# Kernel optimization log

Hardware: AMD Instinct MI355X
Metric: run time of the kernel (lower is better)

Reference implementation:

```python
import jax, jax.numpy as jnp
import numpy as np

GAMMA = 2.0
EPS = 1e-06
LAMBDA_DISTANCE = 1.0
LAMBDA_NORMAL = 0.01
LAMBDA_LAPLACIAN = 0.1
CLS = 1


def vertex_normals(v, f, eps=EPS):
    # v: [N,3], f: [F,3] int. Scatter face normals to vertices, then normalize.
    fv = v[f]  # [F,3,3]
    fn = jnp.cross(fv[:, 1] - fv[:, 0], fv[:, 2] - fv[:, 0])  # [F,3]
    vn = jnp.zeros_like(v)
    vn = vn.at[f[:, 0]].add(fn).at[f[:, 1]].add(fn).at[f[:, 2]].add(fn)
    norm = jnp.maximum(jnp.linalg.norm(vn, axis=-1, keepdims=True), eps)
    return vn / norm


def squared_cdist(a, b):
    # [Na,3] x [Nb,3] -> squared euclidean distances [Na,Nb] (clamped >= 0)
    a2 = jnp.sum(a * a, axis=1)[:, None]
    b2 = jnp.sum(b * b, axis=1)[None, :]
    d2 = a2 + b2 - 2.0 * (a @ b.T)
    return jnp.maximum(d2, 0.0)


def sample_binary_targets(label, v, cls=CLS):
    # Nearest-neighbor grid_sample, align_corners=True, padding zeros.
    # grid = 2*v - 1 -> voxel index = round(v * (size-1)); v[:,0]->W, v[:,1]->H, v[:,2]->D.
    D, H, W = label.shape[2], label.shape[3], label.shape[4]
    ix = jnp.round(v[:, 0] * (W - 1)).astype(jnp.int32)
    iy = jnp.round(v[:, 1] * (H - 1)).astype(jnp.int32)
    iz = jnp.round(v[:, 2] * (D - 1)).astype(jnp.int32)
    inb = (ix >= 0) & (ix < W) & (iy >= 0) & (iy < H) & (iz >= 0) & (iz < D)
    ixc = jnp.clip(ix, 0, W - 1)
    iyc = jnp.clip(iy, 0, H - 1)
    izc = jnp.clip(iz, 0, D - 1)
    vals = (label[0, 0, izc, iyc, ixc] == cls).astype(jnp.float32)
    return jnp.where(inb, vals, 0.0)


def spatial_consistency_loss(rel_pos, targets, gamma=GAMMA, eps=EPS):
    p = jnp.clip(rel_pos, eps, 1.0 - eps)
    pos = targets > 0.5
    pc = jnp.sum(pos).astype(p.dtype)
    tot = jnp.asarray(p.shape[0], p.dtype)
    nc = tot - pc
    alpha = nc / (tot + eps)
    lpos = -alpha * jnp.power(1.0 - p, gamma) * jnp.log(p)
    lneg = -(1.0 - alpha) * jnp.power(p, gamma) * jnp.log(1.0 - p)
    return jnp.sum(jnp.where(pos, lpos, lneg)) / (tot + eps)


def laplacian_uniform(v, f):
    # Uniform mesh Laplacian smoothing: || mean(neighbors) - v ||, averaged.
    i = jnp.concatenate([f[:, 0], f[:, 1], f[:, 2], f[:, 1], f[:, 2], f[:, 0]])
    j = jnp.concatenate([f[:, 1], f[:, 2], f[:, 0], f[:, 0], f[:, 1], f[:, 2]])
    nsum = jnp.zeros_like(v).at[i].add(v[j])
    deg = jnp.zeros((v.shape[0],), v.dtype).at[i].add(1.0)
    lap = nsum / jnp.maximum(deg, 1.0)[:, None] - v
    return jnp.mean(jnp.linalg.norm(lap, axis=1))


def loss_forward(pred_vertices, relative_positions, gt_vertices, pred_faces, gt_faces, label):
    gt_v = jax.lax.stop_gradient(gt_vertices)  # gt comes from label volume; detached in original
    gt_normals = vertex_normals(gt_v, gt_faces)
    # spatial (focal-style) loss
    targets = sample_binary_targets(label, pred_vertices)
    spatial = spatial_consistency_loss(relative_positions, targets)
    # chamfer-style squared surface distance
    d2 = squared_cdist(pred_vertices, gt_v)  # [Np,Ng]
    distance = jnp.mean(jnp.min(d2, axis=1)) + jnp.mean(jnp.min(d2, axis=0))
    # normal consistency vs nearest gt vertex
    pred_normals = vertex_normals(pred_vertices, pred_faces)
    nearest = jnp.argmin(d2, axis=1)
    normal = jnp.mean((pred_normals - gt_normals[nearest]) ** 2)
    # uniform laplacian smoothing
    laplacian = laplacian_uniform(pred_vertices, pred_faces)
    total = spatial + LAMBDA_DISTANCE * distance + LAMBDA_NORMAL * normal + LAMBDA_LAPLACIAN * laplacian
    return total


def setup_inputs() -> dict:
    key = jax.random.key(0)
    k1, k2, k3, k4, k5, k6 = jax.random.split(key, 6)
    Np, Ng = 8192, 12000
    pred_vertices = jax.random.uniform(k1, (Np, 3), dtype=jnp.float32)
    relative_positions = jax.random.uniform(k2, (Np,), dtype=jnp.float32)
    gt_vertices = jax.random.uniform(k3, (Ng, 3), dtype=jnp.float32)
    pred_faces = jax.random.randint(k4, (2 * Np, 3), 0, Np, dtype=jnp.int32)
    gt_faces = jax.random.randint(k5, (2 * Ng, 3), 0, Ng, dtype=jnp.int32)
    label = jax.random.randint(k6, (1, 1, 96, 96, 96), 0, 2, dtype=jnp.int32)
    return {"pred_vertices": pred_vertices, "relative_positions": relative_positions,
            "gt_vertices": gt_vertices, "pred_faces": pred_faces,
            "gt_faces": gt_faces, "label": label}


def reference(pred_vertices, relative_positions, gt_vertices, pred_faces, gt_faces, label):
    return loss_forward(pred_vertices, relative_positions, gt_vertices, pred_faces, gt_faces, label)
```

## Files before the change

kernel.cpp:

```cpp
#include <hip/hip_runtime.h>
#include <math.h>

#define NP 8192
#define NG 12000
#define NFP 16384
#define NFG 24000
#define EPSF 1e-6f

#define GR 16
#define NC (GR*GR*GR)
#define HCELL 0.0625f
#define QL 16
#define QPB (256 / QL)
#define PRED_QBLOCKS (NP / QPB)
#define GT_QBLOCKS (NG / QPB)
#define FIN_TOTAL (PRED_QBLOCKS + GT_QBLOCKS)

static constexpr size_t OFF_STARTP = 0;
static constexpr size_t OFF_CURP   = 16640;
static constexpr size_t OFF_STARTG = 33024;
static constexpr size_t OFF_CURG   = 49664;
static constexpr size_t OFF_SORTP  = 66048;
static constexpr size_t OFF_SORTG  = 197120;
static constexpr size_t OFF_GTN    = 389120;
static constexpr size_t OFF_PNN    = 533120;
static constexpr size_t OFF_NSUM   = 631424;
static constexpr size_t OFF_DEG    = 729728;
static constexpr size_t OFF_PART   = 762496;
#define N_ZERO 93344

__device__ __forceinline__ int cell_of(float x) {
    int c = (int)(x * (float)GR);
    return min(max(c, 0), GR - 1);
}

__device__ __forceinline__ void hist_scan(const float* __restrict__ pts, int n,
                                          unsigned* __restrict__ start,
                                          unsigned* __restrict__ cur,
                                          unsigned* h, unsigned* ps) {
    int t = threadIdx.x;
    for (int i = t; i < NC; i += 1024) h[i] = 0u;
    __syncthreads();
    for (int i = t; i < n; i += 1024) {
        int c = (cell_of(pts[3*i+2]) * GR + cell_of(pts[3*i+1])) * GR + cell_of(pts[3*i]);
        atomicAdd(&h[c], 1u);
    }
    __syncthreads();
    unsigned a0 = h[4*t], a1 = h[4*t+1], a2 = h[4*t+2], a3 = h[4*t+3];
    unsigned tsum = a0 + a1 + a2 + a3;
    ps[t] = tsum; __syncthreads();
    for (int off = 1; off < 1024; off <<= 1) {
        unsigned v = (t >= off) ? ps[t - off] : 0u;
        __syncthreads();
        ps[t] += v;
        __syncthreads();
    }
    unsigned ex = ps[t] - tsum;
    h[4*t] = ex; h[4*t+1] = ex + a0; h[4*t+2] = ex + a0 + a1; h[4*t+3] = ex + a0 + a1 + a2;
    __syncthreads();
    for (int i = t; i < NC; i += 1024) { start[i] = h[i]; cur[i] = h[i]; }
    if (t == 0) start[NC] = (unsigned)n;
}

__global__ __launch_bounds__(1024) void build_kernel(const float* __restrict__ pred,
                                                     const float* __restrict__ gt,
                                                     unsigned* __restrict__ startP,
                                                     unsigned* __restrict__ curP,
                                                     unsigned* __restrict__ startG,
                                                     unsigned* __restrict__ curG,
                                                     float* __restrict__ zero) {
    __shared__ unsigned h[NC];
    __shared__ unsigned ps[1024];
    if (blockIdx.x == 0) {
        hist_scan(pred, NP, startP, curP, h, ps);
    } else if (blockIdx.x == 1) {
        hist_scan(gt, NG, startG, curG, h, ps);
    } else {
        int i = (blockIdx.x - 2) * 1024 + threadIdx.x;
        if (i < N_ZERO) zero[i] = 0.0f;
    }
}

#define SCAT_P_BLOCKS 32
#define SCAT_G_BLOCKS 47
#define SCAT_BLOCKS (SCAT_P_BLOCKS + SCAT_G_BLOCKS)
#define FACE_BLOCKS ((NFG + NFP + 255) / 256)
__global__ __launch_bounds__(256) void scatter_faces_kernel(const float* __restrict__ pred,
                                                            const int* __restrict__ pf,
                                                            const float* __restrict__ gt,
                                                            const int* __restrict__ gf,
                                                            unsigned* __restrict__ curP,
                                                            unsigned* __restrict__ curG,
                                                            float4* __restrict__ sortP,
                                                            float4* __restrict__ sortG,
                                                            float* __restrict__ gtn,
                                                            float* __restrict__ pnn,
                                                            float* __restrict__ nsum,
                                                            float* __restrict__ deg) {
    int b = blockIdx.x;
    if (b < SCAT_P_BLOCKS) {
        int i = b * 256 + threadIdx.x;
        float x = pred[3*i], y = pred[3*i+1], z = pred[3*i+2];
        int c = (cell_of(z) * GR + cell_of(y)) * GR + cell_of(x);
        unsigned pos = atomicAdd(&curP[c], 1u);
        sortP[pos] = make_float4(x, y, z, __int_as_float(i));
    } else if (b < SCAT_BLOCKS) {
        int i = (b - SCAT_P_BLOCKS) * 256 + threadIdx.x;
        if (i < NG) {
            float x = gt[3*i], y = gt[3*i+1], z = gt[3*i+2];
            int c = (cell_of(z) * GR + cell_of(y)) * GR + cell_of(x);
            unsigned pos = atomicAdd(&curG[c], 1u);
            sortG[pos] = make_float4(x, y, z, __int_as_float(i));
        }
    } else {
        int t = (b - SCAT_BLOCKS) * 256 + threadIdx.x;
        if (t < NFG) {
            int i0 = gf[3*t], i1 = gf[3*t+1], i2 = gf[3*t+2];
            float ax = gt[3*i0], ay = gt[3*i0+1], az = gt[3*i0+2];
            float bx = gt[3*i1], by = gt[3*i1+1], bz = gt[3*i1+2];
            float cx = gt[3*i2], cy = gt[3*i2+1], cz = gt[3*i2+2];
            float ux = bx-ax, uy = by-ay, uz = bz-az;
            float wx = cx-ax, wy = cy-ay, wz = cz-az;
            float nx = uy*wz - uz*wy, ny = uz*wx - ux*wz, nz = ux*wy - uy*wx;
            atomicAdd(&gtn[3*i0+0], nx); atomicAdd(&gtn[3*i0+1], ny); atomicAdd(&gtn[3*i0+2], nz);
            atomicAdd(&gtn[3*i1+0], nx); atomicAdd(&gtn[3*i1+1], ny); atomicAdd(&gtn[3*i1+2], nz);
            atomicAdd(&gtn[3*i2+0], nx); atomicAdd(&gtn[3*i2+1], ny); atomicAdd(&gtn[3*i2+2], nz);
        } else if (t < NFG + NFP) {
            int u = t - NFG;
            int i0 = pf[3*u], i1 = pf[3*u+1], i2 = pf[3*u+2];
            float ax = pred[3*i0], ay = pred[3*i0+1], az = pred[3*i0+2];
            float bx = pred[3*i1], by = pred[3*i1+1], bz = pred[3*i1+2];
            float cx = pred[3*i2], cy = pred[3*i2+1], cz = pred[3*i2+2];
            float ux = bx-ax, uy = by-ay, uz = bz-az;
            float wx = cx-ax, wy = cy-ay, wz = cz-az;
            float nx = uy*wz - uz*wy, ny = uz*wx - ux*wz, nz = ux*wy - uy*wx;
            atomicAdd(&pnn[3*i0+0], nx); atomicAdd(&pnn[3*i0+1], ny); atomicAdd(&pnn[3*i0+2], nz);
            atomicAdd(&pnn[3*i1+0], nx); atomicAdd(&pnn[3*i1+1], ny); atomicAdd(&pnn[3*i1+2], nz);
            atomicAdd(&pnn[3*i2+0], nx); atomicAdd(&pnn[3*i2+1], ny); atomicAdd(&pnn[3*i2+2], nz);
            atomicAdd(&nsum[3*i0+0], bx+cx); atomicAdd(&nsum[3*i0+1], by+cy); atomicAdd(&nsum[3*i0+2], bz+cz);
            atomicAdd(&nsum[3*i1+0], cx+ax); atomicAdd(&nsum[3*i1+1], cy+ay); atomicAdd(&nsum[3*i1+2], cz+az);
            atomicAdd(&nsum[3*i2+0], ax+bx); atomicAdd(&nsum[3*i2+1], ay+by); atomicAdd(&nsum[3*i2+2], az+bz);
            atomicAdd(&deg[i0], 2.0f); atomicAdd(&deg[i1], 2.0f); atomicAdd(&deg[i2], 2.0f);
        }
    }
}

__device__ __forceinline__ float wave_sum(float x) {
    #pragma unroll
    for (int o = 32; o > 0; o >>= 1) x += __shfl_down(x, o, 64);
    return x;
}

__device__ __forceinline__ unsigned long long u64min(unsigned long long a,
                                                     unsigned long long b) {
    return a < b ? a : b;
}

__device__ __forceinline__ unsigned long long group_nn(int lane,
                                                       float px, float py, float pz,
                                                       const float4* __restrict__ S,
                                                       const unsigned* __restrict__ cstart) {
    int cx = cell_of(px), cy = cell_of(py), cz = cell_of(pz);
    unsigned long long best = 0xFFFFFFFFFFFFFFFFULL;
    for (int r = 1; ; ++r) {
        int w = 2 * r + 1;
        int nrows = w * w;
        int x0 = max(cx - r, 0), x1 = min(cx + r, GR - 1);
        unsigned long long lb = 0xFFFFFFFFFFFFFFFFULL;
        for (int k = lane; k < nrows; k += QL) {
            int z = cz + k / w - r, y = cy + k % w - r;
            if (z >= 0 && z < GR && y >= 0 && y < GR) {
                int rowbase = (z * GR + y) * GR;
                unsigned s0 = cstart[rowbase + x0];
                unsigned s1 = cstart[rowbase + x1 + 1];
                for (unsigned t = s0; t < s1; ++t) {
                    float4 q = S[t];
                    float ddx = px - q.x, ddy = py - q.y, ddz = pz - q.z;
                    float d2 = fmaf(ddx, ddx, fmaf(ddy, ddy, ddz*ddz));
                    unsigned long long key =
                        ((unsigned long long)__float_as_uint(d2) << 32) |
                        (unsigned)__float_as_int(q.w);
                    lb = u64min(lb, key);
                }
            }
        }
        best = u64min(best, lb);
        #pragma unroll
        for (int m = 1; m < QL; m <<= 1)
            best = u64min(best, (unsigned long long)__shfl_xor((long long)best, m, 64));
        bool covered = (cx - r <= 0) & (cx + r >= GR - 1) &
                       (cy - r <= 0) & (cy + r >= GR - 1) &
                       (cz - r <= 0) & (cz + r >= GR - 1);
        if (covered) break;
        float blo = 1.0e30f;
        if (cx - r > 0)      blo = fminf(blo, px - (float)(cx - r) * HCELL);
        if (cx + r < GR - 1) blo = fminf(blo, (float)(cx + r + 1) * HCELL - px);
        if (cy - r > 0)      blo = fminf(blo, py - (float)(cy - r) * HCELL);
        if (cy + r < GR - 1) blo = fminf(blo, (float)(cy + r + 1) * HCELL - py);
        if (cz - r > 0)      blo = fminf(blo, pz - (float)(cz - r) * HCELL);
        if (cz + r < GR - 1) blo = fminf(blo, (float)(cz + r + 1) * HCELL - pz);
        float bd2 = __uint_as_float((unsigned)(best >> 32));
        if (bd2 <= blo * blo) break;
    }
    return best;
}

__global__ __launch_bounds__(256) void query_kernel(const float* __restrict__ relpos,
                                                    const int* __restrict__ label,
                                                    const float4* __restrict__ sortP,
                                                    const float4* __restrict__ sortG,
                                                    const unsigned* __restrict__ startP,
                                                    const unsigned* __restrict__ startG,
                                                    const float* __restrict__ pnn,
                                                    const float* __restrict__ gtn,
                                                    const float* __restrict__ nsum,
                                                    const float* __restrict__ deg,
                                                    float* __restrict__ partial) {
    __shared__ float bsum[6];
    if (threadIdx.x < 6) bsum[threadIdx.x] = 0.0f;
    __syncthreads();
    int lane = threadIdx.x & (QL - 1);
    int group = threadIdx.x >> 4;
    if (blockIdx.x < PRED_QBLOCKS) {
        int qid = blockIdx.x * QPB + group;
        float4 P = sortP[qid];
        float px = P.x, py = P.y, pz = P.z;
        unsigned long long key = group_nn(lane, px, py, pz, sortG, startG);

        float r0 = 0.f, r1 = 0.f, r2 = 0.f, r3 = 0.f, r4 = 0.f, r5 = 0.f;
        if (lane == 0) {
            int v = __float_as_int(P.w);
            float dmin = __uint_as_float((unsigned)(key >> 32));
            int nearest = (int)(unsigned)(key & 0xffffffffu);

            float ax = pnn[3*v], ay = pnn[3*v+1], az = pnn[3*v+2];
            float an = fmaxf(sqrtf(ax*ax + ay*ay + az*az), EPSF);
            float gx = gtn[3*nearest], gy = gtn[3*nearest+1], gz = gtn[3*nearest+2];
            float gn = fmaxf(sqrtf(gx*gx + gy*gy + gz*gz), EPSF);
            float nx = ax/an - gx/gn, ny = ay/an - gy/gn, nz = az/an - gz/gn;
            float sse = nx*nx + ny*ny + nz*nz;

            float d = fmaxf(deg[v], 1.0f);
            float lx = nsum[3*v]/d - px, ly = nsum[3*v+1]/d - py, lz = nsum[3*v+2]/d - pz;
            float lapn = sqrtf(lx*lx + ly*ly + lz*lz);

            int ix = (int)rintf(px * 95.0f), iy = (int)rintf(py * 95.0f), iz = (int)rintf(pz * 95.0f);
            bool inb = (ix >= 0) & (ix < 96) & (iy >= 0) & (iy < 96) & (iz >= 0) & (iz < 96);
            int ixc = min(max(ix, 0), 95), iyc = min(max(iy, 0), 95), izc = min(max(iz, 0), 95);
            bool pos = inb && (label[(izc*96 + iyc)*96 + ixc] == 1);

            float p = fminf(fmaxf(relpos[v], EPSF), 1.0f - EPSF);
            float om = 1.0f - p;
            float pcnt = 0.0f, sx = 0.0f, sy = 0.0f;
            if (pos) { pcnt = 1.0f; sx = om*om*logf(p); }
            else     { sy = p*p*logf(om); }

            r0 = dmin; r1 = sse; r2 = lapn; r3 = pcnt; r4 = sx; r5 = sy;
        }
        r0 = wave_sum(r0); r1 = wave_sum(r1); r2 = wave_sum(r2);
        r3 = wave_sum(r3); r4 = wave_sum(r4); r5 = wave_sum(r5);
        if ((threadIdx.x & 63) == 0) {
            atomicAdd(&bsum[0], r0); atomicAdd(&bsum[1], r1);
            atomicAdd(&bsum[2], r2); atomicAdd(&bsum[3], r3);
            atomicAdd(&bsum[4], r4); atomicAdd(&bsum[5], r5);
        }
        __syncthreads();
        if (threadIdx.x < 6)
            partial[(size_t)blockIdx.x * 8 + threadIdx.x] = bsum[threadIdx.x];
    } else {
        int qid = (blockIdx.x - PRED_QBLOCKS) * QPB + group;
        float4 Q = sortG[qid];
        unsigned long long key = group_nn(lane, Q.x, Q.y, Q.z, sortP, startP);
        float val = (lane == 0) ? __uint_as_float((unsigned)(key >> 32)) : 0.0f;
        float r = wave_sum(val);
        if ((threadIdx.x & 63) == 0) atomicAdd(&bsum[0], r);
        __syncthreads();
        if (threadIdx.x == 0)
            partial[(size_t)blockIdx.x * 8] = bsum[0];
    }
}

__global__ __launch_bounds__(256) void combine_kernel(const float* __restrict__ partial,
                                                      float* __restrict__ out) {
    float s0=0.f, s1=0.f, s2=0.f, s3=0.f, s4=0.f, s5=0.f, s6=0.f;
    for (int r = threadIdx.x; r < FIN_TOTAL; r += 256) {
        const float* p = partial + (size_t)r * 8;
        if (r < PRED_QBLOCKS) {
            s0 += p[0]; s1 += p[1]; s2 += p[2];
            s3 += p[3]; s4 += p[4]; s5 += p[5];
        } else {
            s6 += p[0];
        }
    }
    s0 = wave_sum(s0); s1 = wave_sum(s1); s2 = wave_sum(s2); s3 = wave_sum(s3);
    s4 = wave_sum(s4); s5 = wave_sum(s5); s6 = wave_sum(s6);
    __shared__ float acc[7];
    if (threadIdx.x < 7) acc[threadIdx.x] = 0.0f;
    __syncthreads();
    if ((threadIdx.x & 63) == 0) {
        atomicAdd(&acc[0], s0); atomicAdd(&acc[1], s1); atomicAdd(&acc[2], s2);
        atomicAdd(&acc[3], s3); atomicAdd(&acc[4], s4); atomicAdd(&acc[5], s5);
        atomicAdd(&acc[6], s6);
    }
    __syncthreads();
    if (threadIdx.x == 0) {
        float sum_row = acc[0], sse = acc[1], lap = acc[2];
        float pc = acc[3], SX = acc[4], SY = acc[5], sum_col = acc[6];
        float tot = (float)NP;
        float alpha = (tot - pc) / (tot + EPSF);
        float spatial = (-alpha * SX - (1.0f - alpha) * SY) / (tot + EPSF);
        float distance = sum_row / (float)NP + sum_col / (float)NG;
        float normal = sse / (float)(NP * 3);
        float lapm = lap / (float)NP;
        out[0] = spatial + 1.0f * distance + 0.01f * normal + 0.1f * lapm;
    }
}

extern "C" void kernel_launch(void* const* d_in, const int* in_sizes, int n_in,
                              void* d_out, int out_size, void* d_ws, size_t ws_size,
                              hipStream_t stream) {
    const float* pred   = (const float*)d_in[0];
    const float* relpos = (const float*)d_in[1];
    const float* gt     = (const float*)d_in[2];
    const int*   pfaces = (const int*)d_in[3];
    const int*   gfaces = (const int*)d_in[4];
    const int*   label  = (const int*)d_in[5];
    float* out = (float*)d_out;

    char* ws = (char*)d_ws;
    unsigned* startP  = (unsigned*)(ws + OFF_STARTP);
    unsigned* curP    = (unsigned*)(ws + OFF_CURP);
    unsigned* startG  = (unsigned*)(ws + OFF_STARTG);
    unsigned* curG    = (unsigned*)(ws + OFF_CURG);
    float4*   sortP   = (float4*)(ws + OFF_SORTP);
    float4*   sortG   = (float4*)(ws + OFF_SORTG);
    float*    gtn     = (float*)(ws + OFF_GTN);
    float*    pnn     = (float*)(ws + OFF_PNN);
    float*    nsum    = (float*)(ws + OFF_NSUM);
    float*    deg     = (float*)(ws + OFF_DEG);
    float*    partial = (float*)(ws + OFF_PART);

    int zero_blocks = (N_ZERO + 1023) / 1024;
    hipLaunchKernelGGL(build_kernel, dim3(2 + zero_blocks), dim3(1024), 0, stream,
                       pred, gt, startP, curP, startG, curG, gtn);
    hipLaunchKernelGGL(scatter_faces_kernel, dim3(SCAT_BLOCKS + FACE_BLOCKS), dim3(256), 0, stream,
                       pred, pfaces, gt, gfaces, curP, curG, sortP, sortG,
                       gtn, pnn, nsum, deg);
    hipLaunchKernelGGL(query_kernel, dim3(FIN_TOTAL), dim3(256), 0, stream,
                       relpos, label, sortP, sortG, startP, startG,
                       pnn, gtn, nsum, deg, partial);
    hipLaunchKernelGGL(combine_kernel, dim3(1), dim3(256), 0, stream, partial, out);
}
```

Measured before the change: 116.3 us.

## Restructure pipeline: scatter in build kernel, overlap face normals with NN queries

The point-to-cell scatter moves into the single-block histogram kernel, using shared-memory atomics on the scanned offsets. Face-normal and Laplacian accumulation now run in the same launch as the nearest-neighbour queries, so the separate scatter kernel goes away. Pred queries only store their NN keys, and a single-block finalize kernel computes the per-vertex normal, Laplacian and focal terms and reduces everything. This cuts the chain from four launches to three, at the cost of serializing the scatter inside one block per cloud and doing 8192 vertex finalizations in one 256-thread block.

After: 176.4 us. 51.6% more time.

```diff
diff --git a/kernel.cpp b/kernel.cpp
--- a/kernel.cpp
+++ b/kernel.cpp
@@ -14,19 +14,17 @@
 #define QPB (256 / QL)
 #define PRED_QBLOCKS (NP / QPB)
 #define GT_QBLOCKS (NG / QPB)
-#define FIN_TOTAL (PRED_QBLOCKS + GT_QBLOCKS)
 
 static constexpr size_t OFF_STARTP = 0;
-static constexpr size_t OFF_CURP   = 16640;
-static constexpr size_t OFF_STARTG = 33024;
-static constexpr size_t OFF_CURG   = 49664;
-static constexpr size_t OFF_SORTP  = 66048;
-static constexpr size_t OFF_SORTG  = 197120;
-static constexpr size_t OFF_GTN    = 389120;
-static constexpr size_t OFF_PNN    = 533120;
-static constexpr size_t OFF_NSUM   = 631424;
-static constexpr size_t OFF_DEG    = 729728;
-static constexpr size_t OFF_PART   = 762496;
+static constexpr size_t OFF_STARTG = 16640;
+static constexpr size_t OFF_SORTP  = 33280;
+static constexpr size_t OFF_SORTG  = 164352;
+static constexpr size_t OFF_KEYS   = 356352;
+static constexpr size_t OFF_COLP   = 421888;
+static constexpr size_t OFF_GTN    = 424960;
+static constexpr size_t OFF_PNN    = 568960;
+static constexpr size_t OFF_NSUM   = 667264;
+static constexpr size_t OFF_DEG    = 765568;
 #define N_ZERO 93344
 
 __device__ __forceinline__ int cell_of(float x) {
@@ -34,10 +32,10 @@
     return min(max(c, 0), GR - 1);
 }
 
-__device__ __forceinline__ void hist_scan(const float* __restrict__ pts, int n,
-                                          unsigned* __restrict__ start,
-                                          unsigned* __restrict__ cur,
-                                          unsigned* h, unsigned* ps) {
+__device__ __forceinline__ void hist_scan_scatter(const float* __restrict__ pts, int n,
+                                                  unsigned* __restrict__ start,
+                                                  float4* __restrict__ sorted,
+                                                  unsigned* h, unsigned* ps) {
     int t = threadIdx.x;
     for (int i = t; i < NC; i += 1024) h[i] = 0u;
     __syncthreads();
@@ -58,90 +56,33 @@
     unsigned ex = ps[t] - tsum;
     h[4*t] = ex; h[4*t+1] = ex + a0; h[4*t+2] = ex + a0 + a1; h[4*t+3] = ex + a0 + a1 + a2;
     __syncthreads();
-    for (int i = t; i < NC; i += 1024) { start[i] = h[i]; cur[i] = h[i]; }
+    for (int i = t; i < NC; i += 1024) start[i] = h[i];
     if (t == 0) start[NC] = (unsigned)n;
+    __syncthreads();
+    for (int i = t; i < n; i += 1024) {
+        float x = pts[3*i], y = pts[3*i+1], z = pts[3*i+2];
+        int c = (cell_of(z) * GR + cell_of(y)) * GR + cell_of(x);
+        unsigned pos = atomicAdd(&h[c], 1u);
+        sorted[pos] = make_float4(x, y, z, __int_as_float(i));
+    }
 }
 
 __global__ __launch_bounds__(1024) void build_kernel(const float* __restrict__ pred,
                                                      const float* __restrict__ gt,
                                                      unsigned* __restrict__ startP,
-                                                     unsigned* __restrict__ curP,
                                                      unsigned* __restrict__ startG,
-                                                     unsigned* __restrict__ curG,
+                                                     float4* __restrict__ sortP,
+                                                     float4* __restrict__ sortG,
                                                      float* __restrict__ zero) {
     __shared__ unsigned h[NC];
     __shared__ unsigned ps[1024];
     if (blockIdx.x == 0) {
-        hist_scan(pred, NP, startP, curP, h, ps);
+        hist_scan_scatter(pred, NP, startP, sortP, h, ps);
     } else if (blockIdx.x == 1) {
-        hist_scan(gt, NG, startG, curG, h, ps);
+        hist_scan_scatter(gt, NG, startG, sortG, h, ps);
     } else {
         int i = (blockIdx.x - 2) * 1024 + threadIdx.x;
         if (i < N_ZERO) zero[i] = 0.0f;
-    }
-}
-
-#define SCAT_P_BLOCKS 32
-#define SCAT_G_BLOCKS 47
-#define SCAT_BLOCKS (SCAT_P_BLOCKS + SCAT_G_BLOCKS)
-#define FACE_BLOCKS ((NFG + NFP + 255) / 256)
-__global__ __launch_bounds__(256) void scatter_faces_kernel(const float* __restrict__ pred,
-                                                            const int* __restrict__ pf,
-                                                            const float* __restrict__ gt,
-                                                            const int* __restrict__ gf,
-                                                            unsigned* __restrict__ curP,
-                                                            unsigned* __restrict__ curG,
-                                                            float4* __restrict__ sortP,
-                                                            float4* __restrict__ sortG,
-                                                            float* __restrict__ gtn,
-                                                            float* __restrict__ pnn,
-                                                            float* __restrict__ nsum,
-                                                            float* __restrict__ deg) {
-    int b = blockIdx.x;
-    if (b < SCAT_P_BLOCKS) {
-        int i = b * 256 + threadIdx.x;
-        float x = pred[3*i], y = pred[3*i+1], z = pred[3*i+2];
-        int c = (cell_of(z) * GR + cell_of(y)) * GR + cell_of(x);
-        unsigned pos = atomicAdd(&curP[c], 1u);
-        sortP[pos] = make_float4(x, y, z, __int_as_float(i));
-    } else if (b < SCAT_BLOCKS) {
-        int i = (b - SCAT_P_BLOCKS) * 256 + threadIdx.x;
-        if (i < NG) {
-            float x = gt[3*i], y = gt[3*i+1], z = gt[3*i+2];
-            int c = (cell_of(z) * GR + cell_of(y)) * GR + cell_of(x);
-            unsigned pos = atomicAdd(&curG[c], 1u);
-            sortG[pos] = make_float4(x, y, z, __int_as_float(i));
-        }
-    } else {
-        int t = (b - SCAT_BLOCKS) * 256 + threadIdx.x;
-        if (t < NFG) {
-            int i0 = gf[3*t], i1 = gf[3*t+1], i2 = gf[3*t+2];
-            float ax = gt[3*i0], ay = gt[3*i0+1], az = gt[3*i0+2];
-            float bx = gt[3*i1], by = gt[3*i1+1], bz = gt[3*i1+2];
-            float cx = gt[3*i2], cy = gt[3*i2+1], cz = gt[3*i2+2];
-            float ux = bx-ax, uy = by-ay, uz = bz-az;
-            float wx = cx-ax, wy = cy-ay, wz = cz-az;
-            float nx = uy*wz - uz*wy, ny = uz*wx - ux*wz, nz = ux*wy - uy*wx;
-            atomicAdd(&gtn[3*i0+0], nx); atomicAdd(&gtn[3*i0+1], ny); atomicAdd(&gtn[3*i0+2], nz);
-            atomicAdd(&gtn[3*i1+0], nx); atomicAdd(&gtn[3*i1+1], ny); atomicAdd(&gtn[3*i1+2], nz);
-            atomicAdd(&gtn[3*i2+0], nx); atomicAdd(&gtn[3*i2+1], ny); atomicAdd(&gtn[3*i2+2], nz);
-        } else if (t < NFG + NFP) {
-            int u = t - NFG;
-            int i0 = pf[3*u], i1 = pf[3*u+1], i2 = pf[3*u+2];
-            float ax = pred[3*i0], ay = pred[3*i0+1], az = pred[3*i0+2];
-            float bx = pred[3*i1], by = pred[3*i1+1], bz = pred[3*i1+2];
-            float cx = pred[3*i2], cy = pred[3*i2+1], cz = pred[3*i2+2];
-            float ux = bx-ax, uy = by-ay, uz = bz-az;
-            float wx = cx-ax, wy = cy-ay, wz = cz-az;
-            float nx = uy*wz - uz*wy, ny = uz*wx - ux*wz, nz = ux*wy - uy*wx;
-            atomicAdd(&pnn[3*i0+0], nx); atomicAdd(&pnn[3*i0+1], ny); atomicAdd(&pnn[3*i0+2], nz);
-            atomicAdd(&pnn[3*i1+0], nx); atomicAdd(&pnn[3*i1+1], ny); atomicAdd(&pnn[3*i1+2], nz);
-            atomicAdd(&pnn[3*i2+0], nx); atomicAdd(&pnn[3*i2+1], ny); atomicAdd(&pnn[3*i2+2], nz);
-            atomicAdd(&nsum[3*i0+0], bx+cx); atomicAdd(&nsum[3*i0+1], by+cy); atomicAdd(&nsum[3*i0+2], bz+cz);
-            atomicAdd(&nsum[3*i1+0], cx+ax); atomicAdd(&nsum[3*i1+1], cy+ay); atomicAdd(&nsum[3*i1+2], cz+az);
-            atomicAdd(&nsum[3*i2+0], ax+bx); atomicAdd(&nsum[3*i2+1], ay+by); atomicAdd(&nsum[3*i2+2], az+bz);
-            atomicAdd(&deg[i0], 2.0f); atomicAdd(&deg[i1], 2.0f); atomicAdd(&deg[i2], 2.0f);
-        }
     }
 }
 
@@ -205,113 +146,139 @@
     return best;
 }
 
-__global__ __launch_bounds__(256) void query_kernel(const float* __restrict__ relpos,
-                                                    const int* __restrict__ label,
-                                                    const float4* __restrict__ sortP,
-                                                    const float4* __restrict__ sortG,
-                                                    const unsigned* __restrict__ startP,
-                                                    const unsigned* __restrict__ startG,
-                                                    const float* __restrict__ pnn,
-                                                    const float* __restrict__ gtn,
-                                                    const float* __restrict__ nsum,
-                                                    const float* __restrict__ deg,
-                                                    float* __restrict__ partial) {
-    __shared__ float bsum[6];
-    if (threadIdx.x < 6) bsum[threadIdx.x] = 0.0f;
-    __syncthreads();
-    int lane = threadIdx.x & (QL - 1);
-    int group = threadIdx.x >> 4;
-    if (blockIdx.x < PRED_QBLOCKS) {
-        int qid = blockIdx.x * QPB + group;
+#define FACE_BLOCKS ((NFG + NFP + 255) / 256)
+#define D2_BLOCKS (FACE_BLOCKS + PRED_QBLOCKS + GT_QBLOCKS)
+__global__ __launch_bounds__(256) void work_kernel(const float* __restrict__ pred,
+                                                   const int* __restrict__ pf,
+                                                   const float* __restrict__ gt,
+                                                   const int* __restrict__ gf,
+                                                   const float4* __restrict__ sortP,
+                                                   const float4* __restrict__ sortG,
+                                                   const unsigned* __restrict__ startP,
+                                                   const unsigned* __restrict__ startG,
+                                                   unsigned long long* __restrict__ keys,
+                                                   float* __restrict__ colpart,
+                                                   float* __restrict__ gtn,
+                                                   float* __restrict__ pnn,
+                                                   float* __restrict__ nsum,
+                                                   float* __restrict__ deg) {
+    int b = blockIdx.x;
+    if (b < FACE_BLOCKS) {
+        int t = b * 256 + threadIdx.x;
+        if (t < NFG) {
+            int i0 = gf[3*t], i1 = gf[3*t+1], i2 = gf[3*t+2];
+            float ax = gt[3*i0], ay = gt[3*i0+1], az = gt[3*i0+2];
+            float bx = gt[3*i1], by = gt[3*i1+1], bz = gt[3*i1+2];
+            float cx = gt[3*i2], cy = gt[3*i2+1], cz = gt[3*i2+2];
+            float ux = bx-ax, uy = by-ay, uz = bz-az;
+            float wx = cx-ax, wy = cy-ay, wz = cz-az;
+            float nx = uy*wz - uz*wy, ny = uz*wx - ux*wz, nz = ux*wy - uy*wx;
+            atomicAdd(&gtn[3*i0+0], nx); atomicAdd(&gtn[3*i0+1], ny); atomicAdd(&gtn[3*i0+2], nz);
+            atomicAdd(&gtn[3*i1+0], nx); atomicAdd(&gtn[3*i1+1], ny); atomicAdd(&gtn[3*i1+2], nz);
+            atomicAdd(&gtn[3*i2+0], nx); atomicAdd(&gtn[3*i2+1], ny); atomicAdd(&gtn[3*i2+2], nz);
+        } else if (t < NFG + NFP) {
+            int u = t - NFG;
+            int i0 = pf[3*u], i1 = pf[3*u+1], i2 = pf[3*u+2];
+            float ax = pred[3*i0], ay = pred[3*i0+1], az = pred[3*i0+2];
+            float bx = pred[3*i1], by = pred[3*i1+1], bz = pred[3*i1+2];
+            float cx = pred[3*i2], cy = pred[3*i2+1], cz = pred[3*i2+2];
+            float ux = bx-ax, uy = by-ay, uz = bz-az;
+            float wx = cx-ax, wy = cy-ay, wz = cz-az;
+            float nx = uy*wz - uz*wy, ny = uz*wx - ux*wz, nz = ux*wy - uy*wx;
+            atomicAdd(&pnn[3*i0+0], nx); atomicAdd(&pnn[3*i0+1], ny); atomicAdd(&pnn[3*i0+2], nz);
+            atomicAdd(&pnn[3*i1+0], nx); atomicAdd(&pnn[3*i1+1], ny); atomicAdd(&pnn[3*i1+2], nz);
+            atomicAdd(&pnn[3*i2+0], nx); atomicAdd(&pnn[3*i2+1], ny); atomicAdd(&pnn[3*i2+2], nz);
+            atomicAdd(&nsum[3*i0+0], bx+cx); atomicAdd(&nsum[3*i0+1], by+cy); atomicAdd(&nsum[3*i0+2], bz+cz);
+            atomicAdd(&nsum[3*i1+0], cx+ax); atomicAdd(&nsum[3*i1+1], cy+ay); atomicAdd(&nsum[3*i1+2], cz+az);
+            atomicAdd(&nsum[3*i2+0], ax+bx); atomicAdd(&nsum[3*i2+1], ay+by); atomicAdd(&nsum[3*i2+2], az+bz);
+            atomicAdd(&deg[i0], 2.0f); atomicAdd(&deg[i1], 2.0f); atomicAdd(&deg[i2], 2.0f);
+        }
+    } else if (b < FACE_BLOCKS + PRED_QBLOCKS) {
+        int lane = threadIdx.x & (QL - 1);
+        int group = threadIdx.x >> 4;
+        int qid = (b - FACE_BLOCKS) * QPB + group;
         float4 P = sortP[qid];
-        float px = P.x, py = P.y, pz = P.z;
-        unsigned long long key = group_nn(lane, px, py, pz, sortG, startG);
-
-        float r0 = 0.f, r1 = 0.f, r2 = 0.f, r3 = 0.f, r4 = 0.f, r5 = 0.f;
-        if (lane == 0) {
-            int v = __float_as_int(P.w);
-            float dmin = __uint_as_float((unsigned)(key >> 32));
-            int nearest = (int)(unsigned)(key & 0xffffffffu);
-
-            float ax = pnn[3*v], ay = pnn[3*v+1], az = pnn[3*v+2];
-            float an = fmaxf(sqrtf(ax*ax + ay*ay + az*az), EPSF);
-            float gx = gtn[3*nearest], gy = gtn[3*nearest+1], gz = gtn[3*nearest+2];
-            float gn = fmaxf(sqrtf(gx*gx + gy*gy + gz*gz), EPSF);
-            float nx = ax/an - gx/gn, ny = ay/an - gy/gn, nz = az/an - gz/gn;
-            float sse = nx*nx + ny*ny + nz*nz;
-
-            float d = fmaxf(deg[v], 1.0f);
-            float lx = nsum[3*v]/d - px, ly = nsum[3*v+1]/d - py, lz = nsum[3*v+2]/d - pz;
-            float lapn = sqrtf(lx*lx + ly*ly + lz*lz);
-
-            int ix = (int)rintf(px * 95.0f), iy = (int)rintf(py * 95.0f), iz = (int)rintf(pz * 95.0f);
-            bool inb = (ix >= 0) & (ix < 96) & (iy >= 0) & (iy < 96) & (iz >= 0) & (iz < 96);
-            int ixc = min(max(ix, 0), 95), iyc = min(max(iy, 0), 95), izc = min(max(iz, 0), 95);
-            bool pos = inb && (label[(izc*96 + iyc)*96 + ixc] == 1);
-
-            float p = fminf(fmaxf(relpos[v], EPSF), 1.0f - EPSF);
-            float om = 1.0f - p;
-            float pcnt = 0.0f, sx = 0.0f, sy = 0.0f;
-            if (pos) { pcnt = 1.0f; sx = om*om*logf(p); }
-            else     { sy = p*p*logf(om); }
-
-            r0 = dmin; r1 = sse; r2 = lapn; r3 = pcnt; r4 = sx; r5 = sy;
-        }
-        r0 = wave_sum(r0); r1 = wave_sum(r1); r2 = wave_sum(r2);
-        r3 = wave_sum(r3); r4 = wave_sum(r4); r5 = wave_sum(r5);
-        if ((threadIdx.x & 63) == 0) {
-            atomicAdd(&bsum[0], r0); atomicAdd(&bsum[1], r1);
-            atomicAdd(&bsum[2], r2); atomicAdd(&bsum[3], r3);
-            atomicAdd(&bsum[4], r4); atomicAdd(&bsum[5], r5);
-        }
+        unsigned long long key = group_nn(lane, P.x, P.y, P.z, sortG, startG);
+        if (lane == 0) keys[qid] = key;
+    } else {
+        __shared__ float bsum;
+        if (threadIdx.x == 0) bsum = 0.0f;
         __syncthreads();
-        if (threadIdx.x < 6)
-            partial[(size_t)blockIdx.x * 8 + threadIdx.x] = bsum[threadIdx.x];
-    } else {
-        int qid = (blockIdx.x - PRED_QBLOCKS) * QPB + group;
+        int lane = threadIdx.x & (QL - 1);
+        int group = threadIdx.x >> 4;
+        int qid = (b - FACE_BLOCKS - PRED_QBLOCKS) * QPB + group;
         float4 Q = sortG[qid];
         unsigned long long key = group_nn(lane, Q.x, Q.y, Q.z, sortP, startP);
         float val = (lane == 0) ? __uint_as_float((unsigned)(key >> 32)) : 0.0f;
         float r = wave_sum(val);
-        if ((threadIdx.x & 63) == 0) atomicAdd(&bsum[0], r);
+        if ((threadIdx.x & 63) == 0) atomicAdd(&bsum, r);
         __syncthreads();
         if (threadIdx.x == 0)
-            partial[(size_t)blockIdx.x * 8] = bsum[0];
-    }
-}
-
-__global__ __launch_bounds__(256) void combine_kernel(const float* __restrict__ partial,
-                                                      float* __restrict__ out) {
-    float s0=0.f, s1=0.f, s2=0.f, s3=0.f, s4=0.f, s5=0.f, s6=0.f;
-    for (int r = threadIdx.x; r < FIN_TOTAL; r += 256) {
-        const float* p = partial + (size_t)r * 8;
-        if (r < PRED_QBLOCKS) {
-            s0 += p[0]; s1 += p[1]; s2 += p[2];
-            s3 += p[3]; s4 += p[4]; s5 += p[5];
-        } else {
-            s6 += p[0];
-        }
-    }
-    s0 = wave_sum(s0); s1 = wave_sum(s1); s2 = wave_sum(s2); s3 = wave_sum(s3);
-    s4 = wave_sum(s4); s5 = wave_sum(s5); s6 = wave_sum(s6);
+            colpart[b - FACE_BLOCKS - PRED_QBLOCKS] = bsum;
+    }
+}
+
+__global__ __launch_bounds__(256) void finalize_kernel(const float* __restrict__ relpos,
+                                                       const int* __restrict__ label,
+                                                       const float4* __restrict__ sortP,
+                                                       const unsigned long long* __restrict__ keys,
+                                                       const float* __restrict__ colpart,
+                                                       const float* __restrict__ pnn,
+                                                       const float* __restrict__ gtn,
+                                                       const float* __restrict__ nsum,
+                                                       const float* __restrict__ deg,
+                                                       float* __restrict__ out) {
+    float s_row = 0.f, s_sse = 0.f, s_lap = 0.f, s_pc = 0.f, s_sx = 0.f, s_sy = 0.f, s_col = 0.f;
+    for (int i = threadIdx.x; i < NP; i += 256) {
+        float4 P = sortP[i];
+        float px = P.x, py = P.y, pz = P.z;
+        int v = __float_as_int(P.w);
+        unsigned long long key = keys[i];
+        s_row += __uint_as_float((unsigned)(key >> 32));
+        int nearest = (int)(unsigned)(key & 0xffffffffu);
+
+        float ax = pnn[3*v], ay = pnn[3*v+1], az = pnn[3*v+2];
+        float an = fmaxf(sqrtf(ax*ax + ay*ay + az*az), EPSF);
+        float gx = gtn[3*nearest], gy = gtn[3*nearest+1], gz = gtn[3*nearest+2];
+        float gn = fmaxf(sqrtf(gx*gx + gy*gy + gz*gz), EPSF);
+        float nx = ax/an - gx/gn, ny = ay/an - gy/gn, nz = az/an - gz/gn;
+        s_sse += nx*nx + ny*ny + nz*nz;
+
+        float d = fmaxf(deg[v], 1.0f);
+        float lx = nsum[3*v]/d - px, ly = nsum[3*v+1]/d - py, lz = nsum[3*v+2]/d - pz;
+        s_lap += sqrtf(lx*lx + ly*ly + lz*lz);
+
+        int ix = (int)rintf(px * 95.0f), iy = (int)rintf(py * 95.0f), iz = (int)rintf(pz * 95.0f);
+        bool inb = (ix >= 0) & (ix < 96) & (iy >= 0) & (iy < 96) & (iz >= 0) & (iz < 96);
+        int ixc = min(max(ix, 0), 95), iyc = min(max(iy, 0), 95), izc = min(max(iz, 0), 95);
+        bool pos = inb && (label[(izc*96 + iyc)*96 + ixc] == 1);
+
+        float p = fminf(fmaxf(relpos[v], EPSF), 1.0f - EPSF);
+        float om = 1.0f - p;
+        if (pos) { s_pc += 1.0f; s_sx += om*om*logf(p); }
+        else     { s_sy += p*p*logf(om); }
+    }
+    for (int j = threadIdx.x; j < GT_QBLOCKS; j += 256) s_col += colpart[j];
+
+    s_row = wave_sum(s_row); s_sse = wave_sum(s_sse); s_lap = wave_sum(s_lap);
+    s_pc = wave_sum(s_pc); s_sx = wave_sum(s_sx); s_sy = wave_sum(s_sy);
+    s_col = wave_sum(s_col);
     __shared__ float acc[7];
     if (threadIdx.x < 7) acc[threadIdx.x] = 0.0f;
     __syncthreads();
     if ((threadIdx.x & 63) == 0) {
-        atomicAdd(&acc[0], s0); atomicAdd(&acc[1], s1); atomicAdd(&acc[2], s2);
-        atomicAdd(&acc[3], s3); atomicAdd(&acc[4], s4); atomicAdd(&acc[5], s5);
-        atomicAdd(&acc[6], s6);
+        atomicAdd(&acc[0], s_row); atomicAdd(&acc[1], s_sse); atomicAdd(&acc[2], s_lap);
+        atomicAdd(&acc[3], s_pc);  atomicAdd(&acc[4], s_sx);  atomicAdd(&acc[5], s_sy);
+        atomicAdd(&acc[6], s_col);
     }
     __syncthreads();
     if (threadIdx.x == 0) {
-        float sum_row = acc[0], sse = acc[1], lap = acc[2];
-        float pc = acc[3], SX = acc[4], SY = acc[5], sum_col = acc[6];
         float tot = (float)NP;
-        float alpha = (tot - pc) / (tot + EPSF);
-        float spatial = (-alpha * SX - (1.0f - alpha) * SY) / (tot + EPSF);
-        float distance = sum_row / (float)NP + sum_col / (float)NG;
-        float normal = sse / (float)(NP * 3);
-        float lapm = lap / (float)NP;
+        float alpha = (tot - acc[3]) / (tot + EPSF);
+        float spatial = (-alpha * acc[4] - (1.0f - alpha) * acc[5]) / (tot + EPSF);
+        float distance = acc[0] / (float)NP + acc[6] / (float)NG;
+        float normal = acc[1] / (float)(NP * 3);
+        float lapm = acc[2] / (float)NP;
         out[0] = spatial + 1.0f * distance + 0.01f * normal + 0.1f * lapm;
     }
 }
@@ -329,25 +296,23 @@
 
     char* ws = (char*)d_ws;
     unsigned* startP  = (unsigned*)(ws + OFF_STARTP);
-    unsigned* curP    = (unsigned*)(ws + OFF_CURP);
     unsigned* startG  = (unsigned*)(ws + OFF_STARTG);
-    unsigned* curG    = (unsigned*)(ws + OFF_CURG);
     float4*   sortP   = (float4*)(ws + OFF_SORTP);
     float4*   sortG   = (float4*)(ws + OFF_SORTG);
+    unsigned long long* keys = (unsigned long long*)(ws + OFF_KEYS);
+    float*    colpart = (float*)(ws + OFF_COLP);
     float*    gtn     = (float*)(ws + OFF_GTN);
     float*    pnn     = (float*)(ws + OFF_PNN);
     float*    nsum    = (float*)(ws + OFF_NSUM);
     float*    deg     = (float*)(ws + OFF_DEG);
-    float*    partial = (float*)(ws + OFF_PART);
 
     int zero_blocks = (N_ZERO + 1023) / 1024;
     hipLaunchKernelGGL(build_kernel, dim3(2 + zero_blocks), dim3(1024), 0, stream,
-                       pred, gt, startP, curP, startG, curG, gtn);
-    hipLaunchKernelGGL(scatter_faces_kernel, dim3(SCAT_BLOCKS + FACE_BLOCKS), dim3(256), 0, stream,
-                       pred, pfaces, gt, gfaces, curP, curG, sortP, sortG,
-                       gtn, pnn, nsum, deg);
-    hipLaunchKernelGGL(query_kernel, dim3(FIN_TOTAL), dim3(256), 0, stream,
-                       relpos, label, sortP, sortG, startP, startG,
-                       pnn, gtn, nsum, deg, partial);
-    hipLaunchKernelGGL(combine_kernel, dim3(1), dim3(256), 0, stream, partial, out);
-}
+                       pred, gt, startP, startG, sortP, sortG, gtn);
+    hipLaunchKernelGGL(work_kernel, dim3(D2_BLOCKS), dim3(256), 0, stream,
+                       pred, pfaces, gt, gfaces, sortP, sortG, startP, startG,
+                       keys, colpart, gtn, pnn, nsum, deg);
+    hipLaunchKernelGGL(finalize_kernel, dim3(1), dim3(256), 0, stream,
+                       relpos, label, sortP, keys, colpart,
+                       pnn, gtn, nsum, deg, out);
+}
```
